# Kernel optimization log

Measured on AMD Instinct MI355X. Metric: run time of the kernel, lower is better.

Reference implementation:

```python
import jax, jax.numpy as jnp
import numpy as np

B, T, H, M, S, E, IN = 8, 2048, 64, 32, 20, 3, 32
EPS = 1e-8  # torch CosineSimilarity eps


def setup_inputs() -> dict:
    key = jax.random.key(0)
    ks = jax.random.split(key, 7)
    return {
        "x": jax.random.normal(ks[0], (B, T, IN), jnp.float32),
        "hidden": jax.random.normal(ks[1], (E, B, T, H), jnp.float32),
        "memory": jax.random.normal(ks[2], (S, M), jnp.float32),
        "Wq": jax.random.normal(ks[3], (E, H, M), jnp.float32),
        "Wk": jax.random.normal(ks[4], (E, H, M), jnp.float32),
        "Wv": jax.random.normal(ks[5], (E, H, M), jnp.float32),
        "input_query": jax.random.normal(ks[6], (IN, M), jnp.float32),
    }


def _cosine(a, b):
    # torch.nn.CosineSimilarity(dim=-1): each vector norm clamped to eps
    na = jnp.maximum(jnp.linalg.norm(a, axis=-1), EPS)
    nb = jnp.maximum(jnp.linalg.norm(b, axis=-1), EPS)
    return jnp.sum(a * b, axis=-1) / (na * nb)


def reference(x, hidden, memory, Wq, Wk, Wv, input_query):
    # query_mem: soft read from global memory slots
    q_in = jnp.einsum('bti,im->btm', x, input_query)           # [B,T,M]
    mem_sc = jax.nn.softmax(jnp.einsum('btm,sm->bts', q_in, memory), axis=-1)
    memories = jnp.einsum('bts,sm->btm', mem_sc, memory)       # [B,T,M]

    # per-expert tiny self-attention (vectorized over expert axis e)
    Q = jnp.einsum('ebth,ehm->ebtm', hidden, Wq)
    K = jnp.einsum('ebth,ehm->ebtm', hidden, Wk)
    V = jnp.einsum('ebth,ehm->ebtm', hidden, Wv)
    energy = jnp.einsum('ebtm,ebsm->ebts', Q, K)               # [E,B,T,T]
    att = jax.nn.softmax(energy, axis=-1)
    out = jnp.einsum('ebts,ebsm->ebtm', att, V)                # [E,B,T,M]

    cos = _cosine(memories[None], out)                         # [E,B,T]
    return jnp.moveaxis(cos, 0, -1)                            # [B,T,E]
```

## Files before the change

kernel.cpp:

```cpp
#include <hip/hip_runtime.h>
#include <hip/hip_bf16.h>

#define Bv  8
#define Tv  2048
#define Hv  64
#define Mv  32
#define Sv  20
#define Ev  3
#define INv 32
#define LOG2E 1.44269504088896340736f

typedef __attribute__((ext_vector_type(8))) _Float16 half8;
typedef __attribute__((ext_vector_type(2))) __fp16 fp16x2;
typedef __attribute__((ext_vector_type(4))) float float4v;

__global__ __launch_bounds__(256) void qkv_kernel(
    const float* __restrict__ hidden,
    const float* __restrict__ Wq,
    const float* __restrict__ Wk,
    const float* __restrict__ Wv,
    const float* __restrict__ x,
    const float* __restrict__ memory,
    const float* __restrict__ iq,
    _Float16* __restrict__ Qh, _Float16* __restrict__ Ql,
    _Float16* __restrict__ Kh, _Float16* __restrict__ Kl,
    _Float16* __restrict__ Vth,
    float* __restrict__ memout)
{
    __shared__ __align__(16) char qsm[43008];
    __shared__ float sIQ[32][32];
    __shared__ float sM[20][32];
    float* sHT = (float*)qsm;
    float* sW  = (float*)(qsm + 17408);

    int bid  = blockIdx.x;
    int tile = bid & 31;
    int b    = (bid >> 5) & 7;
    int e    = bid >> 8;
    int tid  = threadIdx.x;
    size_t eb = (size_t)(e * Bv + b);
    size_t row0 = eb * Tv + (size_t)tile * 64;
    const float* hbase = hidden + row0 * Hv;

    for (int i = tid; i < 32 * 32; i += 256) sIQ[i >> 5][i & 31] = iq[i];
    for (int i = tid; i < 20 * 32; i += 256) sM[i >> 5][i & 31] = memory[i];

    {
        int r  = tid >> 2;
        int c4 = tid & 3;
#pragma unroll
        for (int hh = 0; hh < 4; ++hh) {
            int h4 = c4 + hh * 4;
            float4 v = ((const float4*)(hbase + (size_t)r * Hv))[h4];
            sHT[(h4*4+0)*68 + r] = v.x; sHT[(h4*4+1)*68 + r] = v.y;
            sHT[(h4*4+2)*68 + r] = v.z; sHT[(h4*4+3)*68 + r] = v.w;
        }
    }
    {
        const float* wq = Wq + (size_t)e * Hv * Mv;
        const float* wk = Wk + (size_t)e * Hv * Mv;
        const float* wv = Wv + (size_t)e * Hv * Mv;
        for (int i = tid; i < Hv * Mv; i += 256) {
            int h = i >> 5, m = i & 31;
            sW[h*100 + m]      = wq[i];
            sW[h*100 + 32 + m] = wk[i];
            sW[h*100 + 64 + m] = wv[i];
        }
    }
    __syncthreads();

    int ty = tid >> 4, tx = tid & 15;
    float acc[4][6];
#pragma unroll
    for (int i = 0; i < 4; ++i)
#pragma unroll
        for (int j = 0; j < 6; ++j) acc[i][j] = 0.f;

    for (int h = 0; h < 64; ++h) {
        float4 av = *(const float4*)&sHT[h*68 + ty * 4];
        float a[4] = {av.x, av.y, av.z, av.w};
        float bb[6];
#pragma unroll
        for (int j = 0; j < 6; ++j) bb[j] = sW[h*100 + tx * 6 + j];
#pragma unroll
        for (int i = 0; i < 4; ++i)
#pragma unroll
            for (int j = 0; j < 6; ++j) acc[i][j] = fmaf(a[i], bb[j], acc[i][j]);
    }

    __syncthreads();
    char* sQh = qsm;
    char* sQl = qsm + 4096;
    char* sKh = qsm + 8192;
    char* sKl = qsm + 12288;
    char* sVh = qsm + 16384;
#pragma unroll
    for (int i = 0; i < 4; ++i) {
        int row = ty * 4 + i;
#pragma unroll
        for (int j = 0; j < 6; ++j) {
            int c = tx * 6 + j;
            float v = acc[i][j];
            if (c < 32) {
                v *= LOG2E;
                _Float16 h16 = (_Float16)v;
                _Float16 l16 = (_Float16)(v - (float)h16);
                *(_Float16*)(sQh + row * 64 + c * 2) = h16;
                *(_Float16*)(sQl + row * 64 + c * 2) = l16;
            } else if (c < 64) {
                _Float16 h16 = (_Float16)v;
                _Float16 l16 = (_Float16)(v - (float)h16);
                int m = c - 32, q = m >> 3, wi = m & 7;
                int off = row * 64 + (((q + row) & 3) << 4) + wi * 2;
                *(_Float16*)(sKh + off) = h16;
                *(_Float16*)(sKl + off) = l16;
            } else {
                int d = c - 64, c8 = row >> 3, wi = row & 7;
                int off = d * 128 + (((c8 + d) & 7) << 4) + wi * 2;
                *(_Float16*)(sVh + off) = (_Float16)v;
            }
        }
    }
    __syncthreads();

    size_t pb = eb * (size_t)Tv * 32 + (size_t)tile * 2048;
    _Float16* dsts[5] = {Qh + pb, Ql + pb, Kh + pb, Kl + pb, Vth + pb};
#pragma unroll
    for (int pl = 0; pl < 5; ++pl)
        ((float4*)dsts[pl])[tid] = ((const float4*)(qsm + pl * 4096))[tid];

    if (e == 0 && tid < 64) {
        int t = b * Tv + tile * 64 + tid;
        const float4* xr = (const float4*)(x + (size_t)t * INv);
        float xv[32];
#pragma unroll
        for (int i = 0; i < 8; ++i) {
            float4 v = xr[i];
            xv[4*i] = v.x; xv[4*i+1] = v.y; xv[4*i+2] = v.z; xv[4*i+3] = v.w;
        }
        float qm[32];
#pragma unroll
        for (int m = 0; m < 32; ++m) qm[m] = 0.f;
        for (int i = 0; i < 32; ++i) {
            float xi = xv[i];
#pragma unroll
            for (int m4 = 0; m4 < 8; ++m4) {
                float4 wv = *(const float4*)&sIQ[i][m4 * 4];
                qm[4*m4]   = fmaf(xi, wv.x, qm[4*m4]);
                qm[4*m4+1] = fmaf(xi, wv.y, qm[4*m4+1]);
                qm[4*m4+2] = fmaf(xi, wv.z, qm[4*m4+2]);
                qm[4*m4+3] = fmaf(xi, wv.w, qm[4*m4+3]);
            }
        }
        float sc[20];
#pragma unroll
        for (int j = 0; j < 20; ++j) {
            float a2 = 0.f;
#pragma unroll
            for (int m = 0; m < 32; ++m) a2 = fmaf(qm[m], sM[j][m], a2);
            sc[j] = a2;
        }
        float mx = sc[0];
#pragma unroll
        for (int j = 1; j < 20; ++j) mx = fmaxf(mx, sc[j]);
        float psum = 0.f, p[20];
#pragma unroll
        for (int j = 0; j < 20; ++j) { p[j] = exp2f((sc[j] - mx) * LOG2E); psum += p[j]; }
        float inv = 1.0f / psum;
        float mo[32];
#pragma unroll
        for (int m = 0; m < 32; ++m) mo[m] = 0.f;
        for (int j = 0; j < 20; ++j) {
            float pj = p[j];
#pragma unroll
            for (int m = 0; m < 32; ++m) mo[m] = fmaf(pj, sM[j][m], mo[m]);
        }
        float4* outp = (float4*)(memout + (size_t)t * Mv);
#pragma unroll
        for (int m4 = 0; m4 < 8; ++m4) {
            float4 v;
            v.x = mo[4*m4] * inv; v.y = mo[4*m4+1] * inv;
            v.z = mo[4*m4+2] * inv; v.w = mo[4*m4+3] * inv;
            outp[m4] = v;
        }
    }
}

__device__ __forceinline__ void load_lds16(const _Float16* g, char* l) {
    __builtin_amdgcn_global_load_lds(
        (const __attribute__((address_space(1))) void*)g,
        (__attribute__((address_space(3))) void*)l, 16, 0, 0);
}

__global__ __launch_bounds__(256, 1) void attn_kernel(
    const _Float16* __restrict__ Qh, const _Float16* __restrict__ Ql,
    const _Float16* __restrict__ Kh, const _Float16* __restrict__ Kl,
    const _Float16* __restrict__ Vth,
    const float* __restrict__ memv,
    float* __restrict__ out)
{
    __shared__ __align__(16) char smem[32768];
    const int PW = 24576;

    int bid  = blockIdx.x;
    int xcd  = bid & 7;
    int slot = bid >> 3;
    int tile = slot & 31;
    int ebi  = xcd + ((slot >> 5) << 3);
    int e    = ebi >> 3;
    int b    = ebi & 7;
    int tid  = threadIdx.x;
    int lane = tid & 63;
    int w    = tid >> 6;
    int quad = lane >> 4;
    int l15  = lane & 15;
    size_t eb = (size_t)ebi;
    int q0 = tile * 64 + w * 16;

    size_t qoff = (eb * Tv + (size_t)(q0 + l15)) * 32 + quad * 8;
    half8 qH = *(const half8*)(Qh + qoff);
    half8 qL = *(const half8*)(Ql + qoff);

    float4v O0 = {0.f, 0.f, 0.f, 0.f};
    float4v O1 = {0.f, 0.f, 0.f, 0.f};
    float m_run = -3.0e38f;

    size_t ebOff = eb * (size_t)Tv * 32;
    const _Float16* gp[3] = {Kh + ebOff, Kl + ebOff, Vth + ebOff};

#pragma unroll
    for (int j = 0; j < 3; ++j) {
        int idx = w * 3 + j, p = idx >> 2, k = idx & 3;
        load_lds16(gp[p] + (size_t)k * 512 + lane * 8,
                   smem + p * 4096 + k * 1024);
    }

    for (int c = 0; c < 32; ++c) {
        int pb = c & 1;
        __syncthreads();
        if (c + 1 < 32) {
#pragma unroll
            for (int j = 0; j < 3; ++j) {
                int idx = w * 3 + j, p = idx >> 2, k = idx & 3;
                load_lds16(gp[p] + (size_t)(c + 1) * 2048 + k * 512 + lane * 8,
                           smem + (pb ^ 1) * 12288 + p * 4096 + k * 1024);
            }
        }
        const char* base = smem + pb * 12288;

        float s[16];
        float cmax = -3.0e38f;
#pragma unroll
        for (int tau = 0; tau < 4; ++tau) {
            int r = tau * 16 + l15;
            int sw = ((quad + r) & 3) << 4;
            half8 aH = *(const half8*)(base + r * 64 + sw);
            half8 aL = *(const half8*)(base + 4096 + r * 64 + sw);
            float4v acc = {0.f, 0.f, 0.f, 0.f};
            acc = __builtin_amdgcn_mfma_f32_16x16x32_f16(aH, qL, acc, 0, 0, 0);
            acc = __builtin_amdgcn_mfma_f32_16x16x32_f16(aL, qH, acc, 0, 0, 0);
            acc = __builtin_amdgcn_mfma_f32_16x16x32_f16(aH, qH, acc, 0, 0, 0);
#pragma unroll
            for (int r2 = 0; r2 < 4; ++r2) {
                s[tau * 4 + r2] = acc[r2];
                cmax = fmaxf(cmax, acc[r2]);
            }
        }
        cmax = fmaxf(cmax, __shfl_xor(cmax, 16));
        cmax = fmaxf(cmax, __shfl_xor(cmax, 32));
        float mNew  = fmaxf(m_run, cmax);
        float alpha = exp2f(m_run - mNew);
#pragma unroll
        for (int i = 0; i < 16; ++i)
            s[i] = exp2f(s[i] - mNew);
        m_run = mNew;

#pragma unroll
        for (int r = 0; r < 4; ++r) {
            float ar = __shfl(alpha, quad * 4 + r, 16);
            O0[r] *= ar;
            O1[r] *= ar;
        }

        char* pw = smem + PW + w * 2048 + l15 * 128;
        int xr = l15 & 7;
#pragma unroll
        for (int tau = 0; tau < 4; ++tau) {
            fp16x2 h01 = __builtin_amdgcn_cvt_pkrtz(s[tau*4+0], s[tau*4+1]);
            fp16x2 h23 = __builtin_amdgcn_cvt_pkrtz(s[tau*4+2], s[tau*4+3]);
            uint2 u;
            u.x = __builtin_bit_cast(unsigned int, h01);
            u.y = __builtin_bit_cast(unsigned int, h23);
            int bi = tau * 2 + (quad >> 1);
            *(uint2*)(pw + ((bi ^ xr) << 4) + (quad & 1) * 8) = u;
        }
        __asm__ volatile("" ::: "memory");

#pragma unroll
        for (int ks = 0; ks < 2; ++ks) {
            int swv = ((ks * 4 + quad + l15) & 7) << 4;
            half8 pA  = *(const half8*)(pw + (((ks * 4 + quad) ^ xr) << 4));
            half8 v0H = *(const half8*)(base + 8192 + l15 * 128 + swv);
            half8 v1H = *(const half8*)(base + 8192 + (16 + l15) * 128 + swv);
            O0 = __builtin_amdgcn_mfma_f32_16x16x32_f16(pA, v0H, O0, 0, 0, 0);
            O1 = __builtin_amdgcn_mfma_f32_16x16x32_f16(pA, v1H, O1, 0, 0, 0);
        }
    }

    const float* mb = memv + (size_t)b * Tv * 32;
    float dotr[4], nor[4], nmr[4];
#pragma unroll
    for (int r = 0; r < 4; ++r) {
        int trow = q0 + quad * 4 + r;
        float mv0 = mb[(size_t)trow * 32 + l15];
        float mv1 = mb[(size_t)trow * 32 + 16 + l15];
        float d  = O0[r] * mv0 + O1[r] * mv1;
        float n  = O0[r] * O0[r] + O1[r] * O1[r];
        float nm = mv0 * mv0 + mv1 * mv1;
#pragma unroll
        for (int delta = 1; delta < 16; delta <<= 1) {
            d  += __shfl_xor(d,  delta);
            n  += __shfl_xor(n,  delta);
            nm += __shfl_xor(nm, delta);
        }
        dotr[r] = d; nor[r] = n; nmr[r] = nm;
    }
    if (l15 < 4) {
        int r = l15;
        float na = fmaxf(sqrtf(nmr[r]), 1e-8f);
        float nb = fmaxf(sqrtf(nor[r]), 1e-30f);
        float cosv = dotr[r] / (na * nb);
        int trow = q0 + quad * 4 + r;
        out[((size_t)b * Tv + trow) * Ev + e] = cosv;
    }
}

extern "C" void kernel_launch(void* const* d_in, const int* in_sizes, int n_in,
                              void* d_out, int out_size, void* d_ws, size_t ws_size,
                              hipStream_t stream) {
    const float* x      = (const float*)d_in[0];
    const float* hidden = (const float*)d_in[1];
    const float* memory = (const float*)d_in[2];
    const float* Wq     = (const float*)d_in[3];
    const float* Wk     = (const float*)d_in[4];
    const float* Wv     = (const float*)d_in[5];
    const float* iq     = (const float*)d_in[6];
    float* out          = (float*)d_out;

    char* ws = (char*)d_ws;
    const size_t PLANE = (size_t)Ev * Bv * Tv * 32 * 2;
    float*    memout = (float*)ws;
    _Float16* Qh  = (_Float16*)(ws + 2097152);
    _Float16* Ql  = (_Float16*)(ws + 2097152 + PLANE);
    _Float16* Kh  = (_Float16*)(ws + 2097152 + 2 * PLANE);
    _Float16* Kl  = (_Float16*)(ws + 2097152 + 3 * PLANE);
    _Float16* Vth = (_Float16*)(ws + 2097152 + 4 * PLANE);

    qkv_kernel<<<Ev * Bv * (Tv / 64), 256, 0, stream>>>(hidden, Wq, Wk, Wv,
                                                        x, memory, iq,
                                                        Qh, Ql, Kh, Kl, Vth, memout);
    attn_kernel<<<Ev * Bv * (Tv / 64), 256, 0, stream>>>(Qh, Ql, Kh, Kl, Vth,
                                                         memout, out);
}
```

Baseline: 148.1 us.

## Compute QKV projection with split-fp16 MFMA instead of scalar FMA

Replaces the scalar-FMA 64x96 QKV projection in qkv_kernel with 16x16x32 f16 MFMA instructions. The hidden and weight values are split into hi/lo fp16 parts and combined with three MFMAs to keep near-fp32 accuracy. Hidden rows are loaded straight into registers instead of being transposed through shared memory, and the weights are stored as swizzled fp16 hi/lo in a smaller LDS buffer. This targets the compute and LDS cost of the projection stage, at the price of small rounding differences from the split-precision scheme.

```diff
diff --git a/kernel.cpp b/kernel.cpp
--- a/kernel.cpp
+++ b/kernel.cpp
@@ -27,65 +27,73 @@
     _Float16* __restrict__ Vth,
     float* __restrict__ memout)
 {
-    __shared__ __align__(16) char qsm[43008];
+    __shared__ __align__(16) char qsm[24576];
     __shared__ float sIQ[32][32];
     __shared__ float sM[20][32];
-    float* sHT = (float*)qsm;
-    float* sW  = (float*)(qsm + 17408);
 
     int bid  = blockIdx.x;
     int tile = bid & 31;
     int b    = (bid >> 5) & 7;
     int e    = bid >> 8;
     int tid  = threadIdx.x;
+    int lane = tid & 63;
+    int w    = tid >> 6;
+    int quad = lane >> 4;
+    int l15  = lane & 15;
     size_t eb = (size_t)(e * Bv + b);
-    size_t row0 = eb * Tv + (size_t)tile * 64;
-    const float* hbase = hidden + row0 * Hv;
 
     for (int i = tid; i < 32 * 32; i += 256) sIQ[i >> 5][i & 31] = iq[i];
     for (int i = tid; i < 20 * 32; i += 256) sM[i >> 5][i & 31] = memory[i];
 
-    {
-        int r  = tid >> 2;
-        int c4 = tid & 3;
-#pragma unroll
-        for (int hh = 0; hh < 4; ++hh) {
-            int h4 = c4 + hh * 4;
-            float4 v = ((const float4*)(hbase + (size_t)r * Hv))[h4];
-            sHT[(h4*4+0)*68 + r] = v.x; sHT[(h4*4+1)*68 + r] = v.y;
-            sHT[(h4*4+2)*68 + r] = v.z; sHT[(h4*4+3)*68 + r] = v.w;
-        }
-    }
     {
         const float* wq = Wq + (size_t)e * Hv * Mv;
         const float* wk = Wk + (size_t)e * Hv * Mv;
         const float* wv = Wv + (size_t)e * Hv * Mv;
-        for (int i = tid; i < Hv * Mv; i += 256) {
-            int h = i >> 5, m = i & 31;
-            sW[h*100 + m]      = wq[i];
-            sW[h*100 + 32 + m] = wk[i];
-            sW[h*100 + 64 + m] = wv[i];
+        for (int i = tid; i < 96 * 64; i += 256) {
+            int c = i >> 6, h = i & 63;
+            float v = (c < 32) ? wq[h * 32 + c]
+                    : (c < 64) ? wk[h * 32 + (c - 32)]
+                               : wv[h * 32 + (c - 64)];
+            _Float16 h16 = (_Float16)v;
+            _Float16 l16 = (_Float16)(v - (float)h16);
+            int off = c * 128 + ((((h >> 3) + c) & 7) << 4) + (h & 7) * 2;
+            *(_Float16*)(qsm + off)         = h16;
+            *(_Float16*)(qsm + 12288 + off) = l16;
         }
     }
     __syncthreads();
 
-    int ty = tid >> 4, tx = tid & 15;
-    float acc[4][6];
-#pragma unroll
-    for (int i = 0; i < 4; ++i)
-#pragma unroll
-        for (int j = 0; j < 6; ++j) acc[i][j] = 0.f;
-
-    for (int h = 0; h < 64; ++h) {
-        float4 av = *(const float4*)&sHT[h*68 + ty * 4];
-        float a[4] = {av.x, av.y, av.z, av.w};
-        float bb[6];
-#pragma unroll
-        for (int j = 0; j < 6; ++j) bb[j] = sW[h*100 + tx * 6 + j];
-#pragma unroll
-        for (int i = 0; i < 4; ++i)
-#pragma unroll
-            for (int j = 0; j < 6; ++j) acc[i][j] = fmaf(a[i], bb[j], acc[i][j]);
+    size_t grow = eb * Tv + (size_t)tile * 64 + w * 16 + l15;
+    const float4* hrow = (const float4*)(hidden + grow * Hv);
+    half8 aH[2], aL[2];
+#pragma unroll
+    for (int ks = 0; ks < 2; ++ks) {
+        float4 v0 = hrow[ks * 8 + quad * 2];
+        float4 v1 = hrow[ks * 8 + quad * 2 + 1];
+        float av[8] = {v0.x, v0.y, v0.z, v0.w, v1.x, v1.y, v1.z, v1.w};
+#pragma unroll
+        for (int j = 0; j < 8; ++j) {
+            _Float16 h16 = (_Float16)av[j];
+            aH[ks][j] = h16;
+            aL[ks][j] = (_Float16)(av[j] - (float)h16);
+        }
+    }
+
+    float4v acc[6];
+#pragma unroll
+    for (int nt = 0; nt < 6; ++nt) acc[nt] = (float4v){0.f, 0.f, 0.f, 0.f};
+#pragma unroll
+    for (int ks = 0; ks < 2; ++ks) {
+#pragma unroll
+        for (int nt = 0; nt < 6; ++nt) {
+            int cc = nt * 16 + l15;
+            int sw = (((ks * 4 + quad) + cc) & 7) << 4;
+            half8 bH = *(const half8*)(qsm + cc * 128 + sw);
+            half8 bL = *(const half8*)(qsm + 12288 + cc * 128 + sw);
+            acc[nt] = __builtin_amdgcn_mfma_f32_16x16x32_f16(aH[ks], bL, acc[nt], 0, 0, 0);
+            acc[nt] = __builtin_amdgcn_mfma_f32_16x16x32_f16(aL[ks], bH, acc[nt], 0, 0, 0);
+            acc[nt] = __builtin_amdgcn_mfma_f32_16x16x32_f16(aH[ks], bH, acc[nt], 0, 0, 0);
+        }
     }
 
     __syncthreads();
@@ -95,12 +103,12 @@
     char* sKl = qsm + 12288;
     char* sVh = qsm + 16384;
 #pragma unroll
-    for (int i = 0; i < 4; ++i) {
-        int row = ty * 4 + i;
-#pragma unroll
-        for (int j = 0; j < 6; ++j) {
-            int c = tx * 6 + j;
-            float v = acc[i][j];
+    for (int nt = 0; nt < 6; ++nt) {
+        int c = nt * 16 + l15;
+#pragma unroll
+        for (int r = 0; r < 4; ++r) {
+            int row = w * 16 + quad * 4 + r;
+            float v = acc[nt][r];
             if (c < 32) {
                 v *= LOG2E;
                 _Float16 h16 = (_Float16)v;
```

New measurement: 150.7 us. Within noise of the previous version (+1.8%).
